# Kernel optimization log

Hardware: AMD Instinct MI355X
Metric: run time of the kernel (lower is better)

Reference implementation:

```python
import jax, jax.numpy as jnp
import numpy as np

INV_TEMPERATURE = 0.125  # 1/sqrt(head_dim=64)


def setup_inputs() -> dict:
    key = jax.random.key(0)
    kq, kk, kv, kp, km = jax.random.split(key, 5)
    B, H, S, D = 8, 8, 2048, 64
    q = jax.random.normal(kq, (B, H, S, D), dtype=jnp.float32)
    k = jax.random.normal(kk, (B, H, S, D), dtype=jnp.float32)
    v = jax.random.normal(kv, (B, H, S, D), dtype=jnp.float32)
    pos_scores = jax.random.normal(kp, (1, H, S, S), dtype=jnp.float32)
    mask = jax.random.uniform(km, (1, 1, S, S), dtype=jnp.float32)
    return {"q": q, "k": k, "v": v, "pos_scores": pos_scores, "mask": mask}


def reference(q, k, v, pos_scores, mask):
    # sim = (q k^T) * inv_temp + pos_scores, then multiplicative mask
    sim = jnp.einsum('bhid,bhjd->bhij', q, k) * INV_TEMPERATURE
    sim = mask * (sim + pos_scores)
    attn = jax.nn.softmax(sim, axis=-1)
    out = jnp.einsum('bhij,bhjd->bhid', attn, v)
    return out
```

## Files before the change

### kernel.cpp

```cpp
#include <hip/hip_runtime.h>

constexpr int SEQ = 2048;
constexpr int HD  = 64;
constexpr int NH  = 8;
constexpr int NB  = 8;
constexpr int BM  = 64;
constexpr int BN  = 64;
constexpr int KST = 72;
constexpr float INV_T = 0.125f;
constexpr float LOG2E = 1.4426950408889634f;

typedef __attribute__((ext_vector_type(8))) short bf16x8;
typedef __attribute__((ext_vector_type(8))) short s16x8;
typedef __attribute__((ext_vector_type(4))) short s16x4;
typedef __attribute__((ext_vector_type(4))) float f32x4;

__device__ __forceinline__ short f2bf(float f) {
  unsigned u = __builtin_bit_cast(unsigned, f);
  u += 0x7fffu + ((u >> 16) & 1u);
  return (short)(u >> 16);
}
__device__ __forceinline__ float bf2f(short s) {
  unsigned u = ((unsigned)(unsigned short)s) << 16;
  return __builtin_bit_cast(float, u);
}
__device__ __forceinline__ float fast_exp2(float x) {
#if __has_builtin(__builtin_amdgcn_exp2f)
  return __builtin_amdgcn_exp2f(x);
#else
  return exp2f(x);
#endif
}

__global__ __launch_bounds__(256)
void prep_kv(const float* __restrict__ k, const float* __restrict__ v,
             unsigned short* __restrict__ kb, unsigned short* __restrict__ vt)
{
  __shared__ unsigned short t[HD * KST];
  const int bh = blockIdx.y, jt = blockIdx.x, tid = threadIdx.x;
  const size_t base = (size_t)bh * SEQ * HD + (size_t)jt * BN * HD;

  {
    const float* kp = k + base + 16 * tid;
    unsigned short ko[16];
    for (int e = 0; e < 4; ++e) {
      f32x4 x = *(const f32x4*)(kp + 4 * e);
      for (int c = 0; c < 4; ++c) ko[4 * e + c] = (unsigned short)f2bf(x[c]);
    }
    *(s16x8*)(kb + base + 16 * tid)     = *(const s16x8*)&ko[0];
    *(s16x8*)(kb + base + 16 * tid + 8) = *(const s16x8*)&ko[8];
  }
  {
    const float* vp = v + base + 16 * tid;
    const int j = tid >> 2, d0 = (tid & 3) * 16;
    for (int e = 0; e < 4; ++e) {
      f32x4 x = *(const f32x4*)(vp + 4 * e);
      for (int c = 0; c < 4; ++c) t[(d0 + 4 * e + c) * KST + j] = (unsigned short)f2bf(x[c]);
    }
  }
  __syncthreads();
  {
    const int d = tid >> 2, ch = tid & 3;
    const size_t ob = (size_t)bh * HD * SEQ + (size_t)d * SEQ + jt * BN + ch * 16;
    *(s16x8*)(vt + ob)     = *(const s16x8*)&t[d * KST + ch * 16];
    *(s16x8*)(vt + ob + 8) = *(const s16x8*)&t[d * KST + ch * 16 + 8];
  }
}

__global__ __launch_bounds__(256, 8)
void attn_main(const float* __restrict__ q, const unsigned short* __restrict__ kb,
               const unsigned short* __restrict__ vt,
               const float* __restrict__ pos, const float* __restrict__ mask,
               float* __restrict__ out)
{
  __shared__ unsigned short lds_k[BN * KST];
  __shared__ unsigned short lds_v[HD * KST];

  const int n = blockIdx.x;
  const int x = n & 7, b = (n >> 3) & 7, G = n >> 6;
  const int g = G * 8 + x;
  const int h = g >> 5, it = g & 31;
  const int bh = b * NH + h;
  const int i0 = it * BM;

  const int tid = threadIdx.x, wave = tid >> 6, lane = tid & 63;
  const int quad = lane >> 4, lq = lane & 15;

  bf16x8 aq[2];
  {
    const float* qp = q + ((size_t)bh * SEQ + i0 + wave * 16 + lq) * HD + quad * 8;
    for (int k0 = 0; k0 < 2; ++k0) {
      f32x4 xv = *(const f32x4*)(qp + k0 * 32);
      f32x4 yv = *(const f32x4*)(qp + k0 * 32 + 4);
      for (int c = 0; c < 4; ++c) {
        aq[k0][c]     = f2bf(xv[c] * INV_T);
        aq[k0][4 + c] = f2bf(yv[c] * INV_T);
      }
    }
  }

  f32x4 oacc[4];
  for (int d = 0; d < 4; ++d) oacc[d] = (f32x4){0.f, 0.f, 0.f, 0.f};
  float lrun = 0.f;

  const int lw = (tid >> 3) * KST + (tid & 7) * 8;
  const unsigned short* kgb = kb + (size_t)bh * SEQ * HD + 8 * tid;
  const unsigned short* vgb = vt + (size_t)bh * HD * SEQ + (tid >> 3) * SEQ + (tid & 7) * 8;

  const int irow = i0 + wave * 16 + lq;
  const float* mrow = mask + (size_t)irow * SEQ + quad * 4;
  const float* prow = pos + ((size_t)h * SEQ + irow) * SEQ + quad * 4;

  unsigned short* lds_p = lds_k;
  const int pbase = wave * (16 * KST);

  for (int jt = 0; jt < SEQ / BN; ++jt) {
    __syncthreads();
    s16x8 kx0 = *(const s16x8*)(kgb + jt * 4096);
    s16x8 kx1 = *(const s16x8*)(kgb + jt * 4096 + 2048);
    s16x8 vx0 = *(const s16x8*)(vgb + jt * 64);
    s16x8 vx1 = *(const s16x8*)(vgb + jt * 64 + 32 * SEQ);
    *(s16x8*)&lds_k[lw]            = kx0;
    *(s16x8*)&lds_k[lw + 32 * KST] = kx1;
    *(s16x8*)&lds_v[lw]            = vx0;
    *(s16x8*)&lds_v[lw + 32 * KST] = vx1;
    __syncthreads();

    f32x4 sa[4];
#pragma unroll
    for (int s = 0; s < 4; ++s) sa[s] = (f32x4){0.f, 0.f, 0.f, 0.f};
#pragma unroll
    for (int k0 = 0; k0 < 2; ++k0)
#pragma unroll
      for (int s = 0; s < 4; ++s) {
        bf16x8 bk = *(const bf16x8*)&lds_k[(s * 16 + lq) * KST + k0 * 32 + quad * 8];
        sa[s] = __builtin_amdgcn_mfma_f32_16x16x32_bf16(bk, aq[k0], sa[s], 0, 0, 0);
      }
    __syncthreads();

    const float* mj = mrow + jt * 64;
    const float* pj = prow + jt * 64;
#pragma unroll
    for (int s = 0; s < 4; ++s) {
      f32x4 m4 = *(const f32x4*)(mj + s * 16);
      f32x4 p4 = *(const f32x4*)(pj + s * 16);
      s16x4 pb;
      float ps = 0.f;
#pragma unroll
      for (int r = 0; r < 4; ++r) {
        float t = m4[r] * LOG2E;
        float a = fmaf(t, sa[s][r], t * p4[r]);
        float p = fast_exp2(a);
        unsigned pu = __builtin_bit_cast(unsigned, p);
        pb[r] = (short)(pu >> 16);
        ps += __builtin_bit_cast(float, pu & 0xffff0000u);
      }
      lrun += ps;
      *(s16x4*)&lds_p[pbase + lq * KST + s * 16 + quad * 4] = pb;
    }
    asm volatile("s_waitcnt lgkmcnt(0)" ::: "memory");

#pragma unroll
    for (int k0 = 0; k0 < 2; ++k0) {
      bf16x8 ap = *(const bf16x8*)&lds_p[pbase + lq * KST + k0 * 32 + quad * 8];
#pragma unroll
      for (int d = 0; d < 4; ++d) {
        bf16x8 bv = *(const bf16x8*)&lds_v[(d * 16 + lq) * KST + k0 * 32 + quad * 8];
        oacc[d] = __builtin_amdgcn_mfma_f32_16x16x32_bf16(ap, bv, oacc[d], 0, 0, 0);
      }
    }
  }

  lrun += __shfl_xor(lrun, 16);
  lrun += __shfl_xor(lrun, 32);

#pragma unroll
  for (int r = 0; r < 4; ++r) {
    const float lv = __shfl(lrun, quad * 4 + r);
    const float inv = 1.0f / lv;
    float* orow = out + ((size_t)bh * SEQ + i0 + wave * 16 + quad * 4 + r) * HD + lq;
#pragma unroll
    for (int d = 0; d < 4; ++d) orow[d * 16] = oacc[d][r] * inv;
  }
}

__global__ __launch_bounds__(256, 2)
void attn_fused(const float* __restrict__ q, const float* __restrict__ kk,
                const float* __restrict__ vv, const float* __restrict__ pos,
                const float* __restrict__ mask, float* __restrict__ out)
{
  __shared__ short lds_k[BN * KST];
  __shared__ short lds_v[HD * KST];
  __shared__ short lds_p[4][16 * KST];
  const int bh = blockIdx.y, h = bh & (NH - 1);
  const int i0 = blockIdx.x * BM;
  const int tid = threadIdx.x, wave = tid >> 6, lane = tid & 63;
  const int quad = lane >> 4, lq = lane & 15;
  bf16x8 aq[2];
  {
    const float* qp = q + ((size_t)bh * SEQ + i0 + wave * 16 + lq) * HD + quad * 8;
    for (int k0 = 0; k0 < 2; ++k0) {
      f32x4 xv = *(const f32x4*)(qp + k0 * 32);
      f32x4 yv = *(const f32x4*)(qp + k0 * 32 + 4);
      for (int j = 0; j < 4; ++j) { aq[k0][j] = f2bf(xv[j] * INV_T); aq[k0][4 + j] = f2bf(yv[j] * INV_T); }
    }
  }
  f32x4 oacc[4];
  for (int d = 0; d < 4; ++d) oacc[d] = (f32x4){0.f, 0.f, 0.f, 0.f};
  float mrun[4] = {-INFINITY, -INFINITY, -INFINITY, -INFINITY};
  float lrun[4] = {0.f, 0.f, 0.f, 0.f};
  const size_t kvbase = (size_t)bh * SEQ * HD;
  for (int jt = 0; jt < SEQ / BN; ++jt) {
    const int j0 = jt * BN;
    __syncthreads();
    for (int e = 0; e < 4; ++e) {
      int idx = e * 256 + tid, j = idx >> 4, d4 = (idx & 15) << 2;
      f32x4 kf = *(const f32x4*)(kk + kvbase + (size_t)(j0 + j) * HD + d4);
      s16x4 ks;
      for (int c = 0; c < 4; ++c) ks[c] = f2bf(kf[c]);
      *(s16x4*)&lds_k[j * KST + d4] = ks;
      f32x4 vf = *(const f32x4*)(vv + kvbase + (size_t)(j0 + j) * HD + d4);
      for (int c = 0; c < 4; ++c) lds_v[(d4 + c) * KST + j] = f2bf(vf[c]);
    }
    __syncthreads();
    float mk[4][4], pz[4][4];
    for (int r = 0; r < 4; ++r) {
      const int i = i0 + wave * 16 + quad * 4 + r;
      const float* mrow = mask + (size_t)i * SEQ + j0 + lq;
      const float* prow = pos + ((size_t)h * SEQ + i) * SEQ + j0 + lq;
      for (int s = 0; s < 4; ++s) { mk[r][s] = mrow[s * 16]; pz[r][s] = prow[s * 16]; }
    }
    f32x4 sa[4];
    for (int s = 0; s < 4; ++s) sa[s] = (f32x4){0.f, 0.f, 0.f, 0.f};
    for (int k0 = 0; k0 < 2; ++k0)
      for (int s = 0; s < 4; ++s) {
        bf16x8 bk = *(const bf16x8*)&lds_k[(s * 16 + lq) * KST + k0 * 32 + quad * 8];
        sa[s] = __builtin_amdgcn_mfma_f32_16x16x32_bf16(aq[k0], bk, sa[s], 0, 0, 0);
      }
    for (int r = 0; r < 4; ++r) {
      float s0 = mk[r][0] * (sa[0][r] + pz[r][0]);
      float s1 = mk[r][1] * (sa[1][r] + pz[r][1]);
      float s2 = mk[r][2] * (sa[2][r] + pz[r][2]);
      float s3 = mk[r][3] * (sa[3][r] + pz[r][3]);
      float rm = fmaxf(fmaxf(s0, s1), fmaxf(s2, s3));
      for (int off = 1; off < 16; off <<= 1) rm = fmaxf(rm, __shfl_xor(rm, off));
      float mn = fmaxf(mrun[r], rm);
      float al = __expf(mrun[r] - mn);
      mrun[r] = mn;
      short p0 = f2bf(__expf(s0 - mn)), p1 = f2bf(__expf(s1 - mn));
      short p2 = f2bf(__expf(s2 - mn)), p3 = f2bf(__expf(s3 - mn));
      float ps = bf2f(p0) + bf2f(p1) + bf2f(p2) + bf2f(p3);
      for (int off = 1; off < 16; off <<= 1) ps += __shfl_xor(ps, off);
      lrun[r] = lrun[r] * al + ps;
      for (int d = 0; d < 4; ++d) oacc[d][r] *= al;
      short* pr = &lds_p[wave][(quad * 4 + r) * KST + lq];
      pr[0] = p0; pr[16] = p1; pr[32] = p2; pr[48] = p3;
    }
    asm volatile("s_waitcnt lgkmcnt(0)" ::: "memory");
    for (int k0 = 0; k0 < 2; ++k0) {
      bf16x8 ap = *(const bf16x8*)&lds_p[wave][lq * KST + k0 * 32 + quad * 8];
      for (int d = 0; d < 4; ++d) {
        bf16x8 bv = *(const bf16x8*)&lds_v[(d * 16 + lq) * KST + k0 * 32 + quad * 8];
        oacc[d] = __builtin_amdgcn_mfma_f32_16x16x32_bf16(ap, bv, oacc[d], 0, 0, 0);
      }
    }
  }
  for (int r = 0; r < 4; ++r) {
    const int i = i0 + wave * 16 + quad * 4 + r;
    const float inv = 1.0f / lrun[r];
    float* orow = out + ((size_t)bh * SEQ + i) * HD + lq;
    for (int d = 0; d < 4; ++d) orow[d * 16] = oacc[d][r] * inv;
  }
}

extern "C" void kernel_launch(void* const* d_in, const int* in_sizes, int n_in,
                              void* d_out, int out_size, void* d_ws, size_t ws_size,
                              hipStream_t stream) {
  const float* q    = (const float*)d_in[0];
  const float* k    = (const float*)d_in[1];
  const float* v    = (const float*)d_in[2];
  const float* pos  = (const float*)d_in[3];
  const float* mask = (const float*)d_in[4];
  float* out = (float*)d_out;

  const size_t kv_elems = (size_t)NB * NH * SEQ * HD;
  const size_t kb_bytes = kv_elems * 2;
  const size_t need = 2 * kb_bytes;

  if (ws_size >= need) {
    unsigned short* kb = (unsigned short*)d_ws;
    unsigned short* vt = (unsigned short*)((char*)d_ws + kb_bytes);
    prep_kv<<<dim3(SEQ / BN, NB * NH), dim3(256), 0, stream>>>(k, v, kb, vt);
    attn_main<<<dim3(NB * NH * SEQ / BM), dim3(256), 0, stream>>>(q, kb, vt, pos, mask, out);
  } else {
    attn_fused<<<dim3(SEQ / BM, NB * NH), dim3(256), 0, stream>>>(q, k, v, pos, mask, out);
  }
}
```

Measured before the change: 567.4 us.

## Prefetch next K/V tile and mask/pos values into registers across iterations

Global loads for the next K/V tile and the next mask/pos_scores values are issued into registers during the current iteration, hiding global memory latency behind the MFMA and softmax work. The loop wraps its prefetch index so the final iteration loads tile 0 redundantly instead of branching. Launch bounds drop from 8 to 4 blocks per SM so the extra live registers fit, at the cost of lower occupancy.

Result: faster. 515.7 us (-9.1%).

```diff
diff --git a/kernel.cpp b/kernel.cpp
--- a/kernel.cpp
+++ b/kernel.cpp
@@ -67,7 +67,7 @@
   }
 }
 
-__global__ __launch_bounds__(256, 8)
+__global__ __launch_bounds__(256, 4)
 void attn_main(const float* __restrict__ q, const unsigned short* __restrict__ kb,
                const unsigned short* __restrict__ vt,
                const float* __restrict__ pos, const float* __restrict__ mask,
@@ -114,18 +114,33 @@
   unsigned short* lds_p = lds_k;
   const int pbase = wave * (16 * KST);
 
+  s16x8 kx0, kx1, vx0, vx1;
+  f32x4 m4[4], p4[4];
+
+  kx0 = *(const s16x8*)(kgb);
+  kx1 = *(const s16x8*)(kgb + 2048);
+  vx0 = *(const s16x8*)(vgb);
+  vx1 = *(const s16x8*)(vgb + 32 * SEQ);
+#pragma unroll
+  for (int s = 0; s < 4; ++s) {
+    m4[s] = *(const f32x4*)(mrow + s * 16);
+    p4[s] = *(const f32x4*)(prow + s * 16);
+  }
+
   for (int jt = 0; jt < SEQ / BN; ++jt) {
-    __syncthreads();
-    s16x8 kx0 = *(const s16x8*)(kgb + jt * 4096);
-    s16x8 kx1 = *(const s16x8*)(kgb + jt * 4096 + 2048);
-    s16x8 vx0 = *(const s16x8*)(vgb + jt * 64);
-    s16x8 vx1 = *(const s16x8*)(vgb + jt * 64 + 32 * SEQ);
+    const int jn = (jt + 1) & 31;
+    __syncthreads();
     *(s16x8*)&lds_k[lw]            = kx0;
     *(s16x8*)&lds_k[lw + 32 * KST] = kx1;
     *(s16x8*)&lds_v[lw]            = vx0;
     *(s16x8*)&lds_v[lw + 32 * KST] = vx1;
     __syncthreads();
 
+    kx0 = *(const s16x8*)(kgb + jn * 4096);
+    kx1 = *(const s16x8*)(kgb + jn * 4096 + 2048);
+    vx0 = *(const s16x8*)(vgb + jn * 64);
+    vx1 = *(const s16x8*)(vgb + jn * 64 + 32 * SEQ);
+
     f32x4 sa[4];
 #pragma unroll
     for (int s = 0; s < 4; ++s) sa[s] = (f32x4){0.f, 0.f, 0.f, 0.f};
@@ -138,18 +153,20 @@
       }
     __syncthreads();
 
-    const float* mj = mrow + jt * 64;
-    const float* pj = prow + jt * 64;
+    const float* mjn = mrow + jn * 64;
+    const float* pjn = prow + jn * 64;
 #pragma unroll
     for (int s = 0; s < 4; ++s) {
-      f32x4 m4 = *(const f32x4*)(mj + s * 16);
-      f32x4 p4 = *(const f32x4*)(pj + s * 16);
+      f32x4 mm = m4[s];
+      f32x4 pp = p4[s];
+      m4[s] = *(const f32x4*)(mjn + s * 16);
+      p4[s] = *(const f32x4*)(pjn + s * 16);
       s16x4 pb;
       float ps = 0.f;
 #pragma unroll
       for (int r = 0; r < 4; ++r) {
-        float t = m4[r] * LOG2E;
-        float a = fmaf(t, sa[s][r], t * p4[r]);
+        float t = mm[r] * LOG2E;
+        float a = fmaf(t, sa[s][r], t * pp[r]);
         float p = fast_exp2(a);
         unsigned pu = __builtin_bit_cast(unsigned, p);
         pb[r] = (short)(pu >> 16);
```
